# Performance work log

Hardware: AMD Instinct MI355X
Metric: run time of the kernel (lower is better)

The kernel has to match this reference:

```python
import jax, jax.numpy as jnp
import numpy as np

N_X, N_U, N_Y, HID, T = 1024, 512, 128, 4096, 8192


def setup_inputs() -> dict:
    key = jax.random.key(0)
    ks = jax.random.split(key, 6)
    s = lambda fan_in: 1.0 / np.sqrt(fan_in)
    return {
        "x0": jax.random.normal(ks[0], (N_X,), jnp.float32),
        "u": jax.random.normal(ks[1], (T, N_U), jnp.float32),
        "f_w1": jax.random.normal(ks[2], (N_X + N_U, HID), jnp.float32) * s(N_X + N_U),
        "f_b1": jnp.zeros((HID,), jnp.float32),
        "f_w2": jax.random.normal(ks[3], (HID, N_X), jnp.float32) * s(HID),
        "f_b2": jnp.zeros((N_X,), jnp.float32),
        "g_w1": jax.random.normal(ks[4], (N_X, HID), jnp.float32) * s(N_X),
        "g_b1": jnp.zeros((HID,), jnp.float32),
        "g_w2": jax.random.normal(ks[5], (HID, N_Y), jnp.float32) * s(HID),
        "g_b2": jnp.zeros((N_Y,), jnp.float32),
    }


def reference(x0, u, f_w1, f_b1, f_w2, f_b2, g_w1, g_b1, g_w2, g_b2):
    # Simulator: scan over time; each step:
    #   xu = concat(x, u_t); new_x = f_xu(xu); y_t = g_x(x)
    def step(x, u_t):
        xu = jnp.concatenate([x, u_t])                       # [n_x + n_u]
        new_x = jnp.tanh(xu @ f_w1 + f_b1) @ f_w2 + f_b2     # [n_x]
        y_t = jnp.tanh(x @ g_w1 + g_b1) @ g_w2 + g_b2        # [n_y]
        return new_x, y_t

    _, y = jax.lax.scan(step, x0, u)                         # y: [T, n_y]
    return y
```

## Files before the change

kernel.cpp:

```cpp
#include <hip/hip_runtime.h>
#include <hip/hip_bf16.h>
#include <stdint.h>

#define T_STEPS 8192
#define NX 1024
#define NU 512
#define NY 128
#define HID 4096

#define SEQ_WGS 256
#define SEQ_BLK 512
#define RING 128

typedef __attribute__((ext_vector_type(8))) short bf16x8;
typedef __attribute__((ext_vector_type(4))) float f32x4;
typedef __attribute__((ext_vector_type(2))) short s16x2;

__device__ __forceinline__ float bf2f(ushort u) {
  union { uint32_t i; float f; } v; v.i = ((uint32_t)u) << 16; return v.f;
}
__device__ __forceinline__ ushort f2bf(float f) {
  union { float f; uint32_t i; } v; v.f = f;
  uint32_t r = v.i + 0x7fffu + ((v.i >> 16) & 1u);
  return (ushort)(r >> 16);
}
__device__ __forceinline__ float lof(uint32_t u) {
  union { uint32_t i; float f; } v; v.i = u << 16; return v.f;
}
__device__ __forceinline__ float hif(uint32_t u) {
  union { uint32_t i; float f; } v; v.i = u & 0xffff0000u; return v.f;
}

__device__ __forceinline__ float dot2bf(uint32_t h, uint32_t m, float acc) {
#if __has_builtin(__builtin_amdgcn_fdot2_f32_bf16)
  return __builtin_amdgcn_fdot2_f32_bf16(__builtin_bit_cast(s16x2, h),
                                         __builtin_bit_cast(s16x2, m), acc, false);
#else
  acc = fmaf(lof(h), lof(m), acc);
  return fmaf(hif(h), hif(m), acc);
#endif
}

__device__ __forceinline__ void fixw(uint32_t& x, uint32_t* wp, uint32_t tg) {
  while ((x & 0xffffu) != tg)
    x = __hip_atomic_load(wp, __ATOMIC_RELAXED, __HIP_MEMORY_SCOPE_AGENT);
}


__global__ void cvt_bf16_kernel(const float* __restrict__ in, ushort* __restrict__ out, int n) {
  int i = blockIdx.x * blockDim.x + threadIdx.x;
  int stride = gridDim.x * blockDim.x;
  for (; i < n; i += stride) out[i] = f2bf(in[i]);
}

__global__ void transpose_cvt_kernel(const float* __restrict__ in, ushort* __restrict__ out,
                                     int R, int C) {
  __shared__ float tile[32][33];
  int bx = blockIdx.x, by = blockIdx.y;
  int tx = threadIdx.x, ty = threadIdx.y;
#pragma unroll
  for (int yy = 0; yy < 4; ++yy) {
    long r = (long)by * 32 + ty + yy * 8;
    long c = (long)bx * 32 + tx;
    tile[ty + yy * 8][tx] = in[r * C + c];
  }
  __syncthreads();
#pragma unroll
  for (int yy = 0; yy < 4; ++yy) {
    long c = (long)bx * 32 + ty + yy * 8;
    long r = (long)by * 32 + tx;
    out[c * R + r] = f2bf(tile[tx][ty + yy * 8]);
  }
}

__global__ void bias_dh_kernel(const float* __restrict__ fw1, const float* __restrict__ fb1,
                               const float* __restrict__ fb2, float* __restrict__ biasDH) {
  int j = blockIdx.x * blockDim.x + threadIdx.x;
  float s = fb1[j];
  for (int k = 0; k < NX; ++k) s += fb2[k] * fw1[(long)k * HID + j];
  biasDH[j] = s;
}

__global__ void fixup_row0_kernel(const float* __restrict__ fw1, const float* __restrict__ fb1,
                                  const float* __restrict__ u, const float* __restrict__ x0,
                                  ushort* __restrict__ DH, uint32_t* __restrict__ HTAG) {
  int j = blockIdx.x * blockDim.x + threadIdx.x;
  float s = fb1[j];
  for (int k = 0; k < NU; ++k) s += u[k] * fw1[(long)(NX + k) * HID + j];
  for (int k = 0; k < NX; ++k) s += x0[k] * fw1[(long)k * HID + j];
  float h = tanhf(s);
  ushort hb = f2bf(h);
  DH[j] = hb;
  HTAG[j] = ((uint32_t)hb << 16);
}

__global__ void x0_row_kernel(const float* __restrict__ x0, ushort* __restrict__ X) {
  int j = blockIdx.x * blockDim.x + threadIdx.x;
  if (j < NX) X[j] = f2bf(x0[j]);
}

#define GBM 128
#define GBN 128
#define GBK 32
#define LDT 40

__global__ __launch_bounds__(256) void gemm_kernel(
    const ushort* __restrict__ A, const ushort* __restrict__ BT,
    void* __restrict__ Cout, const float* __restrict__ bias,
    int M, int N, int K, int flags)
{
  __shared__ ushort Al[GBM * LDT];
  __shared__ ushort Bl[GBN * LDT];
  const int tid = threadIdx.x;
  const int bm = blockIdx.y, bn = blockIdx.x;
  const int wave = tid >> 6, lane = tid & 63;
  const int wr = wave >> 1, wc = wave & 1;
  const int l15 = lane & 15, l4 = lane >> 4;

  f32x4 acc[4][4];
#pragma unroll
  for (int m = 0; m < 4; ++m)
#pragma unroll
    for (int n = 0; n < 4; ++n) acc[m][n] = (f32x4){0.f, 0.f, 0.f, 0.f};

  const int r_t = tid >> 1;
  const int h_t = (tid & 1) * 16;
  const long arow = (long)bm * GBM + r_t;
  const long brow = (long)bn * GBN + r_t;

  for (int k0 = 0; k0 < K; k0 += GBK) {
    uint4 a0 = make_uint4(0,0,0,0), a1 = make_uint4(0,0,0,0);
    if (arow < M) {
      const ushort* p = A + arow * K + k0 + h_t;
      a0 = *(const uint4*)p;
      a1 = *(const uint4*)(p + 8);
    }
    const ushort* q = BT + brow * K + k0 + h_t;
    uint4 b0 = *(const uint4*)q;
    uint4 b1 = *(const uint4*)(q + 8);
    __syncthreads();
    *(uint4*)&Al[r_t * LDT + h_t]     = a0;
    *(uint4*)&Al[r_t * LDT + h_t + 8] = a1;
    *(uint4*)&Bl[r_t * LDT + h_t]     = b0;
    *(uint4*)&Bl[r_t * LDT + h_t + 8] = b1;
    __syncthreads();

    bf16x8 af[4], bfv[4];
#pragma unroll
    for (int m = 0; m < 4; ++m)
      af[m] = *(const bf16x8*)&Al[(wr * 64 + m * 16 + l15) * LDT + l4 * 8];
#pragma unroll
    for (int n = 0; n < 4; ++n)
      bfv[n] = *(const bf16x8*)&Bl[(wc * 64 + n * 16 + l15) * LDT + l4 * 8];
#pragma unroll
    for (int m = 0; m < 4; ++m)
#pragma unroll
      for (int n = 0; n < 4; ++n)
        acc[m][n] = __builtin_amdgcn_mfma_f32_16x16x32_bf16(af[m], bfv[n], acc[m][n], 0, 0, 0);
  }

  const bool f32out = (flags & 2) != 0;
  const bool dotanh = (flags & 1) != 0;
#pragma unroll
  for (int m = 0; m < 4; ++m) {
#pragma unroll
    for (int n = 0; n < 4; ++n) {
#pragma unroll
      for (int j = 0; j < 4; ++j) {
        long grow = (long)bm * GBM + wr * 64 + m * 16 + l4 * 4 + j;
        int  gcol = bn * GBN + wc * 64 + n * 16 + l15;
        if (grow < M) {
          float v = acc[m][n][j];
          if (bias) v += bias[gcol];
          if (dotanh) v = tanhf(v);
          if (f32out) ((float*)Cout)[grow * N + gcol] = v;
          else        ((ushort*)Cout)[grow * N + gcol] = f2bf(v);
        }
      }
    }
  }
}

__global__ __launch_bounds__(SEQ_BLK, 1) void seq_kernel(
    const ushort* __restrict__ MT, ushort* __restrict__ DH,
    uint32_t* __restrict__ HTAG, int nsteps)
{
  __shared__ ushort hl[HID];
  const int tid = threadIdx.x;
  const int w = tid >> 6;
  const int lane = tid & 63;
  const int c0 = (blockIdx.x << 4) + (w << 1);

  uint4 mA[8], mB[8];
  {
    const uint4* rA = (const uint4*)(MT + (size_t)c0 * HID);
    const uint4* rB = (const uint4*)(MT + (size_t)(c0 + 1) * HID);
#pragma unroll
    for (int j = 0; j < 8; ++j) {
      mA[j] = rA[lane + 64 * j];
      mB[j] = rB[lane + 64 * j];
    }
  }

  const bool prod = (lane == 0);

  for (int i = 0; i < nsteps; ++i) {
    const uint32_t tg = (uint32_t)i & 0xffffu;
    uint32_t* rowp = HTAG + (size_t)(i & (RING - 1)) * HID;

    float dA = 0.f, dB = 0.f;
    if (prod) {
      uint32_t dw = *(const uint32_t*)(DH + (size_t)(i + 1) * HID + c0);
      dA = lof(dw); dB = hif(dw);
    }

    if (tid < SEQ_WGS) {
      uint32_t* sp = rowp + tid * 16 + 15;
      while ((__hip_atomic_load(sp, __ATOMIC_RELAXED, __HIP_MEMORY_SCOPE_AGENT)
              & 0xffffu) != tg)
        __builtin_amdgcn_s_sleep(1);
    }
    __syncthreads();

    {
      const uint4* rv = (const uint4*)rowp;
      uint4 v0 = rv[tid];
      uint4 v1 = rv[tid + 512];
      uint32_t bad0 = ((v0.x ^ tg) | (v0.y ^ tg) | (v0.z ^ tg) | (v0.w ^ tg)) & 0xffffu;
      if (__builtin_expect(bad0 != 0, 0)) {
        uint32_t* wp = rowp + tid * 4;
        fixw(v0.x, wp + 0, tg); fixw(v0.y, wp + 1, tg);
        fixw(v0.z, wp + 2, tg); fixw(v0.w, wp + 3, tg);
      }
      uint32_t bad1 = ((v1.x ^ tg) | (v1.y ^ tg) | (v1.z ^ tg) | (v1.w ^ tg)) & 0xffffu;
      if (__builtin_expect(bad1 != 0, 0)) {
        uint32_t* wp = rowp + tid * 4 + 2048;
        fixw(v1.x, wp + 0, tg); fixw(v1.y, wp + 1, tg);
        fixw(v1.z, wp + 2, tg); fixw(v1.w, wp + 3, tg);
      }
      unsigned long long* hl64 = (unsigned long long*)hl;
      uint32_t p0 = (v0.x >> 16) | (v0.y & 0xffff0000u);
      uint32_t p1 = (v0.z >> 16) | (v0.w & 0xffff0000u);
      hl64[tid] = ((unsigned long long)p1 << 32) | p0;
      p0 = (v1.x >> 16) | (v1.y & 0xffff0000u);
      p1 = (v1.z >> 16) | (v1.w & 0xffff0000u);
      hl64[tid + 512] = ((unsigned long long)p1 << 32) | p0;
    }
    __syncthreads();

    float accA = 0.f, accB = 0.f;
    const uint4* h4 = (const uint4*)hl;
#pragma unroll
    for (int j = 0; j < 8; ++j) {
      uint4 hv = h4[lane + 64 * j];
      accA = dot2bf(hv.x, mA[j].x, accA);
      accB = dot2bf(hv.x, mB[j].x, accB);
      accA = dot2bf(hv.y, mA[j].y, accA);
      accB = dot2bf(hv.y, mB[j].y, accB);
      accA = dot2bf(hv.z, mA[j].z, accA);
      accB = dot2bf(hv.z, mB[j].z, accB);
      accA = dot2bf(hv.w, mA[j].w, accA);
      accB = dot2bf(hv.w, mB[j].w, accB);
    }
    accA += __shfl_xor(accA, 32, 64);
    accB += __shfl_xor(accB, 32, 64);
    float y = (lane < 32) ? accA : accB;
#pragma unroll
    for (int off = 16; off >= 1; off >>= 1)
      y += __shfl_xor(y, off, 64);
    float totB = __shfl(y, 32, 64);

    if (prod) {
      ushort ha = f2bf(tanhf(y + dA));
      ushort hb = f2bf(tanhf(totB + dB));
      uint32_t tg1 = (uint32_t)(i + 1) & 0xffffu;
      unsigned long long word =
          ((unsigned long long)(((uint32_t)hb << 16) | tg1) << 32) |
          (unsigned long long)(((uint32_t)ha << 16) | tg1);
      unsigned long long* dst =
          (unsigned long long*)(HTAG + (size_t)((i + 1) & (RING - 1)) * HID) + (c0 >> 1);
      __hip_atomic_store(dst, word, __ATOMIC_RELAXED, __HIP_MEMORY_SCOPE_AGENT);
      *(uint32_t*)(DH + (size_t)(i + 1) * HID + c0) = (uint32_t)ha | ((uint32_t)hb << 16);
    }
  }
}


extern "C" void kernel_launch(void* const* d_in, const int* in_sizes, int n_in,
                              void* d_out, int out_size, void* d_ws, size_t ws_size,
                              hipStream_t stream) {
  const float* x0  = (const float*)d_in[0];
  const float* u   = (const float*)d_in[1];
  const float* fw1 = (const float*)d_in[2];
  const float* fb1 = (const float*)d_in[3];
  const float* fw2 = (const float*)d_in[4];
  const float* fb2 = (const float*)d_in[5];
  const float* gw1 = (const float*)d_in[6];
  const float* gb1 = (const float*)d_in[7];
  const float* gw2 = (const float*)d_in[8];
  const float* gb2 = (const float*)d_in[9];
  float* out = (float*)d_out;

  char* ws = (char*)d_ws;
  size_t off = 0;
  auto alloc = [&](size_t bytes) -> char* {
    char* p = ws + off; off += (bytes + 255) & ~(size_t)255; return p;
  };
  ushort* MT     = (ushort*)alloc((size_t)HID * HID * 2);
  ushort* DH     = (ushort*)alloc((size_t)T_STEPS * HID * 2);
  ushort* X      = (ushort*)alloc((size_t)T_STEPS * NX * 2);
  ushort* W1xT   = (ushort*)alloc((size_t)HID * NX * 2);
  ushort* W1uT   = (ushort*)alloc((size_t)HID * NU * 2);
  ushort* W2bf   = (ushort*)alloc((size_t)HID * NX * 2);
  ushort* W2T    = (ushort*)alloc((size_t)NX * HID * 2);
  ushort* Gw1T   = (ushort*)alloc((size_t)HID * NX * 2);
  ushort* Gw2T   = (ushort*)alloc((size_t)NY * HID * 2);
  ushort* Ubf    = (ushort*)alloc((size_t)T_STEPS * NU * 2);
  float*  biasDH = (float*)alloc((size_t)HID * 4);
  uint32_t* HTAG = (uint32_t*)alloc((size_t)RING * HID * 4);
  if (off > ws_size) return;

  cvt_bf16_kernel<<<2048, 256, 0, stream>>>(u, Ubf, T_STEPS * NU);
  cvt_bf16_kernel<<<2048, 256, 0, stream>>>(fw2, W2bf, HID * NX);
  transpose_cvt_kernel<<<dim3(HID/32, NX/32), dim3(32, 8), 0, stream>>>(fw1, W1xT, NX, HID);
  transpose_cvt_kernel<<<dim3(HID/32, NU/32), dim3(32, 8), 0, stream>>>(fw1 + (size_t)NX * HID, W1uT, NU, HID);
  transpose_cvt_kernel<<<dim3(NX/32, HID/32), dim3(32, 8), 0, stream>>>(fw2, W2T, HID, NX);
  transpose_cvt_kernel<<<dim3(HID/32, NX/32), dim3(32, 8), 0, stream>>>(gw1, Gw1T, NX, HID);
  transpose_cvt_kernel<<<dim3(NY/32, HID/32), dim3(32, 8), 0, stream>>>(gw2, Gw2T, HID, NY);
  bias_dh_kernel<<<HID/256, 256, 0, stream>>>(fw1, fb1, fb2, biasDH);

  gemm_kernel<<<dim3(HID/128, HID/128), 256, 0, stream>>>(W1xT, W2bf, MT, nullptr, HID, HID, NX, 0);
  gemm_kernel<<<dim3(HID/128, T_STEPS/128), 256, 0, stream>>>(Ubf, W1uT, DH, biasDH, T_STEPS, HID, NU, 0);
  fixup_row0_kernel<<<HID/256, 256, 0, stream>>>(fw1, fb1, u, x0, DH, HTAG);

  {
    int nsteps = T_STEPS - 2;
    void* MT_p = (void*)MT; void* DH_p = (void*)DH; void* ht_p = (void*)HTAG;
    void* args[] = { &MT_p, &DH_p, &ht_p, &nsteps };
    hipError_t e = hipLaunchCooperativeKernel((const void*)seq_kernel, dim3(SEQ_WGS),
                                              dim3(SEQ_BLK), args, 0, stream);
    if (e != hipSuccess) {
      (void)hipGetLastError();
      seq_kernel<<<SEQ_WGS, SEQ_BLK, 0, stream>>>(MT, DH, HTAG, nsteps);
    }
  }

  x0_row_kernel<<<NX/256, 256, 0, stream>>>(x0, X);
  gemm_kernel<<<dim3(NX/128, T_STEPS/128), 256, 0, stream>>>(DH, W2T, X + NX, fb2, T_STEPS - 1, NX, HID, 0);
  gemm_kernel<<<dim3(HID/128, T_STEPS/128), 256, 0, stream>>>(X, Gw1T, DH, gb1, T_STEPS, HID, NX, 1);
  gemm_kernel<<<dim3(NY/128, T_STEPS/128), 256, 0, stream>>>(DH, Gw2T, out, gb2, T_STEPS, NY, HID, 2);
}
```

Before: 18.93 ms.

## Replace per-step block barriers with per-wave polling and LDS flag handoff

Each wave now polls its own slice of the tagged hidden-state ring with cache-bypassing loads, instead of having a subset of threads spin on sentinel words and then crossing two __syncthreads. The wave publishes its slice to a double-buffered LDS array and signals it with a workgroup-scope release flag, and other waves spin on those flags to consume slices in rotated order. The goal is to remove the full-block barrier latency from the serial recurrence critical path. It also swaps tanhf for an exp2/rcp approximation, which costs some accuracy and adds the risk of LDS spin-wait ordering problems.

```diff
diff --git a/kernel.cpp b/kernel.cpp
--- a/kernel.cpp
+++ b/kernel.cpp
@@ -41,9 +41,24 @@
 #endif
 }
 
+__device__ __forceinline__ float fast_tanh(float x) {
+  float cx = fminf(fmaxf(x, -15.f), 15.f);
+  float e = __builtin_amdgcn_exp2f(cx * 2.8853900817779268f);
+  return 1.f - 2.f * __builtin_amdgcn_rcpf(e + 1.f);
+}
+
 __device__ __forceinline__ void fixw(uint32_t& x, uint32_t* wp, uint32_t tg) {
   while ((x & 0xffffu) != tg)
     x = __hip_atomic_load(wp, __ATOMIC_RELAXED, __HIP_MEMORY_SCOPE_AGENT);
+}
+
+__device__ __forceinline__ void load2_b128_bypass(const uint32_t* p0, uint4& r0, uint4& r1) {
+  asm volatile("global_load_dwordx4 %0, %2, off sc0 sc1\n\t"
+               "global_load_dwordx4 %1, %3, off sc0 sc1\n\t"
+               "s_waitcnt vmcnt(0)"
+               : "=&v"(r0), "=&v"(r1)
+               : "v"(p0), "v"(p0 + 4)
+               : "memory");
 }
 
 
@@ -185,7 +200,9 @@
     const ushort* __restrict__ MT, ushort* __restrict__ DH,
     uint32_t* __restrict__ HTAG, int nsteps)
 {
-  __shared__ ushort hl[HID];
+  __shared__ ushort hl[2][HID];
+  __shared__ int flags[8];
+
   const int tid = threadIdx.x;
   const int w = tid >> 6;
   const int lane = tid & 63;
@@ -202,11 +219,15 @@
     }
   }
 
+  if (tid < 8) flags[tid] = -1;
+  __syncthreads();
+
   const bool prod = (lane == 0);
 
   for (int i = 0; i < nsteps; ++i) {
     const uint32_t tg = (uint32_t)i & 0xffffu;
     uint32_t* rowp = HTAG + (size_t)(i & (RING - 1)) * HID;
+    const int buf = i & 1;
 
     float dA = 0.f, dB = 0.f;
     if (prod) {
@@ -214,54 +235,53 @@
       dA = lof(dw); dB = hif(dw);
     }
 
-    if (tid < SEQ_WGS) {
-      uint32_t* sp = rowp + tid * 16 + 15;
-      while ((__hip_atomic_load(sp, __ATOMIC_RELAXED, __HIP_MEMORY_SCOPE_AGENT)
-              & 0xffffu) != tg)
+    uint32_t* p0 = rowp + 512 * w + 8 * lane;
+    uint4 v0, v1;
+    {
+      int spins = 0;
+      for (;;) {
+        load2_b128_bypass(p0, v0, v1);
+        uint32_t bad = ((v0.x ^ tg) | (v0.y ^ tg) | (v0.z ^ tg) | (v0.w ^ tg) |
+                        (v1.x ^ tg) | (v1.y ^ tg) | (v1.z ^ tg) | (v1.w ^ tg)) & 0xffffu;
+        if (__all(bad == 0)) break;
+        if (__builtin_expect(++spins > (1 << 18), 0)) {
+          fixw(v0.x, p0 + 0, tg); fixw(v0.y, p0 + 1, tg);
+          fixw(v0.z, p0 + 2, tg); fixw(v0.w, p0 + 3, tg);
+          fixw(v1.x, p0 + 4, tg); fixw(v1.y, p0 + 5, tg);
+          fixw(v1.z, p0 + 6, tg); fixw(v1.w, p0 + 7, tg);
+          break;
+        }
         __builtin_amdgcn_s_sleep(1);
-    }
-    __syncthreads();
-
-    {
-      const uint4* rv = (const uint4*)rowp;
-      uint4 v0 = rv[tid];
-      uint4 v1 = rv[tid + 512];
-      uint32_t bad0 = ((v0.x ^ tg) | (v0.y ^ tg) | (v0.z ^ tg) | (v0.w ^ tg)) & 0xffffu;
-      if (__builtin_expect(bad0 != 0, 0)) {
-        uint32_t* wp = rowp + tid * 4;
-        fixw(v0.x, wp + 0, tg); fixw(v0.y, wp + 1, tg);
-        fixw(v0.z, wp + 2, tg); fixw(v0.w, wp + 3, tg);
       }
-      uint32_t bad1 = ((v1.x ^ tg) | (v1.y ^ tg) | (v1.z ^ tg) | (v1.w ^ tg)) & 0xffffu;
-      if (__builtin_expect(bad1 != 0, 0)) {
-        uint32_t* wp = rowp + tid * 4 + 2048;
-        fixw(v1.x, wp + 0, tg); fixw(v1.y, wp + 1, tg);
-        fixw(v1.z, wp + 2, tg); fixw(v1.w, wp + 3, tg);
-      }
-      unsigned long long* hl64 = (unsigned long long*)hl;
-      uint32_t p0 = (v0.x >> 16) | (v0.y & 0xffff0000u);
-      uint32_t p1 = (v0.z >> 16) | (v0.w & 0xffff0000u);
-      hl64[tid] = ((unsigned long long)p1 << 32) | p0;
-      p0 = (v1.x >> 16) | (v1.y & 0xffff0000u);
-      p1 = (v1.z >> 16) | (v1.w & 0xffff0000u);
-      hl64[tid + 512] = ((unsigned long long)p1 << 32) | p0;
-    }
-    __syncthreads();
+    }
+
+    uint4 pk;
+    pk.x = (v0.x >> 16) | (v0.y & 0xffff0000u);
+    pk.y = (v0.z >> 16) | (v0.w & 0xffff0000u);
+    pk.z = (v1.x >> 16) | (v1.y & 0xffff0000u);
+    pk.w = (v1.z >> 16) | (v1.w & 0xffff0000u);
+
+    *(uint4*)&hl[buf][512 * w + 8 * lane] = pk;
+    __hip_atomic_store(&flags[w], i, __ATOMIC_RELEASE, __HIP_MEMORY_SCOPE_WORKGROUP);
 
     float accA = 0.f, accB = 0.f;
-    const uint4* h4 = (const uint4*)hl;
-#pragma unroll
-    for (int j = 0; j < 8; ++j) {
-      uint4 hv = h4[lane + 64 * j];
-      accA = dot2bf(hv.x, mA[j].x, accA);
-      accB = dot2bf(hv.x, mB[j].x, accB);
-      accA = dot2bf(hv.y, mA[j].y, accA);
-      accB = dot2bf(hv.y, mB[j].y, accB);
-      accA = dot2bf(hv.z, mA[j].z, accA);
-      accB = dot2bf(hv.z, mB[j].z, accB);
-      accA = dot2bf(hv.w, mA[j].w, accA);
-      accB = dot2bf(hv.w, mB[j].w, accB);
-    }
+    accA = dot2bf(pk.x, mA[w].x, accA);  accB = dot2bf(pk.x, mB[w].x, accB);
+    accA = dot2bf(pk.y, mA[w].y, accA);  accB = dot2bf(pk.y, mB[w].y, accB);
+    accA = dot2bf(pk.z, mA[w].z, accA);  accB = dot2bf(pk.z, mB[w].z, accB);
+    accA = dot2bf(pk.w, mA[w].w, accA);  accB = dot2bf(pk.w, mB[w].w, accB);
+
+#pragma unroll
+    for (int jj = 1; jj < 8; ++jj) {
+      const int j = (w + jj) & 7;
+      while (__hip_atomic_load(&flags[j], __ATOMIC_ACQUIRE,
+                               __HIP_MEMORY_SCOPE_WORKGROUP) < i) { }
+      uint4 hv = *(const uint4*)&hl[buf][512 * j + 8 * lane];
+      accA = dot2bf(hv.x, mA[j].x, accA);  accB = dot2bf(hv.x, mB[j].x, accB);
+      accA = dot2bf(hv.y, mA[j].y, accA);  accB = dot2bf(hv.y, mB[j].y, accB);
+      accA = dot2bf(hv.z, mA[j].z, accA);  accB = dot2bf(hv.z, mB[j].z, accB);
+      accA = dot2bf(hv.w, mA[j].w, accA);  accB = dot2bf(hv.w, mB[j].w, accB);
+    }
+
     accA += __shfl_xor(accA, 32, 64);
     accB += __shfl_xor(accB, 32, 64);
     float y = (lane < 32) ? accA : accB;
@@ -271,8 +291,8 @@
     float totB = __shfl(y, 32, 64);
 
     if (prod) {
-      ushort ha = f2bf(tanhf(y + dA));
-      ushort hb = f2bf(tanhf(totB + dB));
+      ushort ha = f2bf(fast_tanh(y + dA));
+      ushort hb = f2bf(fast_tanh(totB + dB));
       uint32_t tg1 = (uint32_t)(i + 1) & 0xffffu;
       unsigned long long word =
           ((unsigned long long)(((uint32_t)hb << 16) | tg1) << 32) |
```

New measurement: 64.56 ms. +241.0%, slower.
